# Performance work log

Measured on AMD Instinct MI355X. Metric: run time of the kernel, lower is better.

The kernel has to match this reference:

```python
import jax, jax.numpy as jnp
import numpy as np

NUM_CLASSES = 16
P = 0.8      # mitigation exponent
Q = 2.0      # compensation exponent
EPS = 0.01   # divisor smoothing
IGNORE_INDEX = 0


def setup_inputs() -> dict:
    key = jax.random.key(0)
    k1, k2 = jax.random.split(key)
    cls_score = jax.random.normal(k1, (8, NUM_CLASSES, 512, 512), dtype=jnp.float32)
    labels = jax.random.randint(k2, (8, 512, 512), 0, NUM_CLASSES, dtype=jnp.int32)
    cum_samples = jnp.zeros((NUM_CLASSES,), dtype=jnp.float32)  # persistent buffer, starts at zero
    return {"cls_score": cls_score, "labels": labels, "cum_samples": cum_samples}


def reference(cls_score, labels, cum_samples):
    C = cls_score.shape[1]
    labels = labels.reshape(-1)                                   # [M]
    logits = jnp.transpose(cls_score, (0, 2, 3, 1)).reshape(-1, C)  # [M, C]

    # buffer update: single scatter-add replaces the per-unique-label python loop
    cum = cum_samples.at[labels].add(1.0)                          # [C]
    cum_c = jnp.clip(cum, 1.0, None)

    # mitigation factor: ratio matrix over classes, gathered per pixel label
    ratio = cum_c[None, :] / cum_c[:, None]                        # [C, C]
    mit = jnp.where(ratio < 1.0, ratio ** P, 1.0)                  # [C, C]
    mitigation = mit[labels]                                       # [M, C]

    # compensation factor: detached softmax scores vs self-score
    scores = jax.nn.softmax(jax.lax.stop_gradient(logits), axis=1)  # [M, C]
    self_s = jnp.take_along_axis(scores, labels[:, None], axis=1)   # [M, 1]
    score_mat = scores / jnp.clip(self_s, EPS, None)                # [M, C]
    compensation = jnp.where(score_mat > 1.0, score_mat ** Q, 1.0)  # [M, C]

    seesaw_w = mitigation * compensation                            # [M, C]
    onehot = jax.nn.one_hot(labels, C, dtype=logits.dtype)          # [M, C]
    adj_logits = logits + jnp.log(seesaw_w) * (1.0 - onehot)        # [M, C]

    # CrossEntropyLoss(ignore_index=IGNORE_INDEX, reduction='mean')
    logp = jax.nn.log_softmax(adj_logits, axis=1)
    nll = -jnp.take_along_axis(logp, labels[:, None], axis=1)[:, 0]  # [M]
    mask = (labels != IGNORE_INDEX).astype(logits.dtype)
    loss = jnp.sum(nll * mask) / jnp.sum(mask)
    return loss
```

## Files before the change

kernel.cpp:

```cpp
#include <hip/hip_runtime.h>


constexpr int   kC      = 16;
constexpr int   kHW     = 512 * 512;
constexpr float kP      = 0.8f;
constexpr float kLogEps = -4.605170185988091f;
constexpr int   kNAcc   = 64;

__global__ __launch_bounds__(256) void init_ws_k(unsigned int* ws) {
    for (int i = threadIdx.x; i < 256 + kNAcc * 16; i += 256) ws[i] = 0u;
}

__global__ __launch_bounds__(256) void hist_k(const int4* __restrict__ lab4,
                                              unsigned int* __restrict__ histp) {
    int base = blockIdx.x * 1024 + threadIdx.x;
    int4 v[4];
    #pragma unroll
    for (int j = 0; j < 4; ++j) v[j] = lab4[base + j * 256];
    int cnt[16];
    #pragma unroll
    for (int c = 0; c < 16; ++c) cnt[c] = 0;
    #pragma unroll
    for (int j = 0; j < 4; ++j) {
        #pragma unroll
        for (int c = 0; c < 16; ++c)
            cnt[c] += (v[j].x == c) + (v[j].y == c) + (v[j].z == c) + (v[j].w == c);
    }
    #pragma unroll
    for (int c = 0; c < 16; ++c) {
        int x = cnt[c];
        #pragma unroll
        for (int off = 32; off > 0; off >>= 1) x += __shfl_down(x, off);
        cnt[c] = x;
    }
    __shared__ unsigned int sh[4 * 16];
    int wave = threadIdx.x >> 6, lane = threadIdx.x & 63;
    if (lane == 0) {
        #pragma unroll
        for (int c = 0; c < 16; ++c) sh[wave * 16 + c] = (unsigned)cnt[c];
    }
    __syncthreads();
    int t = threadIdx.x;
    if (t < 16)
        atomicAdd(&histp[t * 16], sh[t] + sh[16 + t] + sh[32 + t] + sh[48 + t]);
}

__global__ __launch_bounds__(256, 6) void seesaw_k(const float* __restrict__ cls,
                                                   const int*   __restrict__ labels,
                                                   const float* __restrict__ cum_in,
                                                   const unsigned int* __restrict__ histp,
                                                   float* __restrict__ ws) {
    __shared__ float s_plog[16];
    __shared__ float s_red[8];
    int t = threadIdx.x;
    if (t < 16) {
        float cc = fmaxf((float)histp[t * 16] + cum_in[t], 1.0f);
        s_plog[t] = kP * __logf(cc);
    }
    __syncthreads();

    long long m0 = (long long)(blockIdx.x * 256 + t) * 2;
    int b  = (int)(m0 >> 18);
    int hw = (int)(m0 & (kHW - 1));
    const float* pbase = cls + (long long)b * kC * kHW + hw;

    float2 lv[16];
    #pragma unroll
    for (int c = 0; c < 16; ++c)
        lv[c] = *(const float2*)(pbase + (long long)c * kHW);
    const int2 lab2 = *(const int2*)(labels + m0);

    float pl[16];
    #pragma unroll
    for (int c = 0; c < 16; ++c) pl[c] = s_plog[c];

    int labs[2] = {lab2.x, lab2.y};

    float lsum = 0.0f, lcnt = 0.0f;
    #pragma unroll
    for (int p = 0; p < 2; ++p) {
        float l[16];
        #pragma unroll
        for (int c = 0; c < 16; ++c) l[c] = ((const float*)&lv[c])[p];
        int lab = labs[p];

        float m1 = l[0];
        float llab = l[0];
        #pragma unroll
        for (int c = 1; c < 16; ++c) {
            m1 = fmaxf(m1, l[c]);
            if (c == lab) llab = l[c];
        }
        float s = 0.0f;
        #pragma unroll
        for (int c = 0; c < 16; ++c) s += __expf(l[c] - m1);
        float K = fmaxf(llab, m1 + __logf(s) + kLogEps);
        float plab = s_plog[lab];

        float m2 = -3.0e38f;
        #pragma unroll
        for (int c = 0; c < 16; ++c) {
            float a = l[c] + fminf(0.0f, pl[c] - plab)
                           + fmaxf(0.0f, 2.0f * (l[c] - K));
            l[c] = a;
            m2 = fmaxf(m2, a);
        }
        float s2 = 0.0f;
        #pragma unroll
        for (int c = 0; c < 16; ++c) s2 += __expf(l[c] - m2);
        float nll = m2 + __logf(s2) - llab;
        if (lab != 0) { lsum += nll; lcnt += 1.0f; }
    }

    #pragma unroll
    for (int off = 32; off > 0; off >>= 1) {
        lsum += __shfl_down(lsum, off);
        lcnt += __shfl_down(lcnt, off);
    }
    int wave = t >> 6, lane = t & 63;
    if (lane == 0) { s_red[wave] = lsum; s_red[4 + wave] = lcnt; }
    __syncthreads();
    if (t == 0) {
        float* pair = ws + 256 + (blockIdx.x & (kNAcc - 1)) * 16;
        atomicAdd(&pair[0], s_red[0] + s_red[1] + s_red[2] + s_red[3]);
        atomicAdd(&pair[1], s_red[4] + s_red[5] + s_red[6] + s_red[7]);
    }
}

__global__ void final_k(const float* __restrict__ ws, float* __restrict__ out) {
    int t = threadIdx.x;
    float a = (t < kNAcc) ? ws[256 + t * 16]     : 0.0f;
    float b = (t < kNAcc) ? ws[256 + t * 16 + 1] : 0.0f;
    #pragma unroll
    for (int off = 32; off > 0; off >>= 1) {
        a += __shfl_down(a, off);
        b += __shfl_down(b, off);
    }
    if (t == 0) out[0] = a / b;
}

extern "C" void kernel_launch(void* const* d_in, const int* in_sizes, int n_in,
                              void* d_out, int out_size, void* d_ws, size_t ws_size,
                              hipStream_t stream) {
    const float* cls    = (const float*)d_in[0];
    const int*   labels = (const int*)d_in[1];
    const float* cum_in = (const float*)d_in[2];
    float* out = (float*)d_out;
    unsigned int* ws = (unsigned int*)d_ws;

    int M  = in_sizes[1];
    int n4 = M / 4;

    init_ws_k<<<1, 256, 0, stream>>>(ws);
    hist_k<<<n4 / 1024, 256, 0, stream>>>((const int4*)labels, ws);
    seesaw_k<<<M / 512, 256, 0, stream>>>(cls, labels, cum_in, ws, (float*)ws);
    final_k<<<1, 64, 0, stream>>>((const float*)ws, out);
}
```

Baseline: 210.7 us.

## Split seesaw loss into per-pixel NLL kernel and separate reduction kernel

The main kernel now handles four pixels per thread with 128-bit nontemporal loads, permutes the block order with a multiplicative hash, and writes per-pixel masked NLL values to workspace. A new kernel then sums those values and the nonzero-label counts with the same atomic accumulation scheme. The aim is wider memory transactions and no reduction or atomic tail in the bandwidth-bound kernel. In exchange it adds a full write and re-read of an M-float buffer, an extra launch and a second pass over labels, and it lowers the occupancy hint from 6 to 4.

```diff
diff --git a/kernel.cpp b/kernel.cpp
--- a/kernel.cpp
+++ b/kernel.cpp
@@ -1,11 +1,15 @@
 #include <hip/hip_runtime.h>
 
+
+typedef float vf4 __attribute__((ext_vector_type(4)));
+typedef int   vi4 __attribute__((ext_vector_type(4)));
 
 constexpr int   kC      = 16;
 constexpr int   kHW     = 512 * 512;
 constexpr float kP      = 0.8f;
 constexpr float kLogEps = -4.605170185988091f;
 constexpr int   kNAcc   = 64;
+constexpr int   kNllOff = 2048;
 
 __global__ __launch_bounds__(256) void init_ws_k(unsigned int* ws) {
     for (int i = threadIdx.x; i < 256 + kNAcc * 16; i += 256) ws[i] = 0u;
@@ -45,13 +49,12 @@
         atomicAdd(&histp[t * 16], sh[t] + sh[16 + t] + sh[32 + t] + sh[48 + t]);
 }
 
-__global__ __launch_bounds__(256, 6) void seesaw_k(const float* __restrict__ cls,
-                                                   const int*   __restrict__ labels,
-                                                   const float* __restrict__ cum_in,
-                                                   const unsigned int* __restrict__ histp,
-                                                   float* __restrict__ ws) {
+__global__ __launch_bounds__(256, 4) void seesawA_k(const float* __restrict__ cls,
+                                                    const int*   __restrict__ labels,
+                                                    const float* __restrict__ cum_in,
+                                                    const unsigned int* __restrict__ histp,
+                                                    float* __restrict__ nll_out) {
     __shared__ float s_plog[16];
-    __shared__ float s_red[8];
     int t = threadIdx.x;
     if (t < 16) {
         float cc = fmaxf((float)histp[t * 16] + cum_in[t], 1.0f);
@@ -59,29 +62,30 @@
     }
     __syncthreads();
 
-    long long m0 = (long long)(blockIdx.x * 256 + t) * 2;
+    int bid = (int)((blockIdx.x * 997u) & 2047u);
+    long long m0 = (long long)(bid * 256 + t) * 4;
     int b  = (int)(m0 >> 18);
     int hw = (int)(m0 & (kHW - 1));
     const float* pbase = cls + (long long)b * kC * kHW + hw;
 
-    float2 lv[16];
+    vf4 lv[16];
     #pragma unroll
     for (int c = 0; c < 16; ++c)
-        lv[c] = *(const float2*)(pbase + (long long)c * kHW);
-    const int2 lab2 = *(const int2*)(labels + m0);
+        lv[c] = __builtin_nontemporal_load((const vf4*)(pbase + (long long)c * kHW));
+    const vi4 lab4 = __builtin_nontemporal_load((const vi4*)(labels + m0));
 
     float pl[16];
     #pragma unroll
     for (int c = 0; c < 16; ++c) pl[c] = s_plog[c];
 
-    int labs[2] = {lab2.x, lab2.y};
+    int labs[4] = {lab4[0], lab4[1], lab4[2], lab4[3]};
+    vf4 nll4;
 
-    float lsum = 0.0f, lcnt = 0.0f;
     #pragma unroll
-    for (int p = 0; p < 2; ++p) {
+    for (int p = 0; p < 4; ++p) {
         float l[16];
         #pragma unroll
-        for (int c = 0; c < 16; ++c) l[c] = ((const float*)&lv[c])[p];
+        for (int c = 0; c < 16; ++c) l[c] = lv[c][p];
         int lab = labs[p];
 
         float m1 = l[0];
@@ -109,18 +113,29 @@
         #pragma unroll
         for (int c = 0; c < 16; ++c) s2 += __expf(l[c] - m2);
         float nll = m2 + __logf(s2) - llab;
-        if (lab != 0) { lsum += nll; lcnt += 1.0f; }
+        nll4[p] = (lab != 0) ? nll : 0.0f;
     }
+    __builtin_nontemporal_store(nll4, (vf4*)(nll_out + m0));
+}
 
+__global__ __launch_bounds__(256) void reduceB_k(const float* __restrict__ nll,
+                                                 const int*   __restrict__ labels,
+                                                 float* __restrict__ ws) {
+    long long m0 = (long long)(blockIdx.x * 256 + threadIdx.x) * 4;
+    const vf4 n4 = *(const vf4*)(nll + m0);
+    const vi4 l4 = *(const vi4*)(labels + m0);
+    float lsum = n4[0] + n4[1] + n4[2] + n4[3];
+    float lcnt = (float)((l4[0] != 0) + (l4[1] != 0) + (l4[2] != 0) + (l4[3] != 0));
     #pragma unroll
     for (int off = 32; off > 0; off >>= 1) {
         lsum += __shfl_down(lsum, off);
         lcnt += __shfl_down(lcnt, off);
     }
-    int wave = t >> 6, lane = t & 63;
+    __shared__ float s_red[8];
+    int wave = threadIdx.x >> 6, lane = threadIdx.x & 63;
     if (lane == 0) { s_red[wave] = lsum; s_red[4 + wave] = lcnt; }
     __syncthreads();
-    if (t == 0) {
+    if (threadIdx.x == 0) {
         float* pair = ws + 256 + (blockIdx.x & (kNAcc - 1)) * 16;
         atomicAdd(&pair[0], s_red[0] + s_red[1] + s_red[2] + s_red[3]);
         atomicAdd(&pair[1], s_red[4] + s_red[5] + s_red[6] + s_red[7]);
@@ -147,12 +162,14 @@
     const float* cum_in = (const float*)d_in[2];
     float* out = (float*)d_out;
     unsigned int* ws = (unsigned int*)d_ws;
+    float* nll = (float*)ws + kNllOff;
 
     int M  = in_sizes[1];
     int n4 = M / 4;
 
     init_ws_k<<<1, 256, 0, stream>>>(ws);
     hist_k<<<n4 / 1024, 256, 0, stream>>>((const int4*)labels, ws);
-    seesaw_k<<<M / 512, 256, 0, stream>>>(cls, labels, cum_in, ws, (float*)ws);
+    seesawA_k<<<M / 1024, 256, 0, stream>>>(cls, labels, cum_in, ws, nll);
+    reduceB_k<<<M / 1024, 256, 0, stream>>>(nll, labels, (float*)ws);
     final_k<<<1, 64, 0, stream>>>((const float*)ws, out);
 }
```

Result: no change. 214.7 us (+1.9%).
